# Kernel tuning notes

Measured on AMD Instinct MI355X. Metric: run time of the kernel, lower is better.

## Reference

```python
import jax, jax.numpy as jnp
import numpy as np

B, S, D, HD, P = 4, 8192, 1024, 128, 32
EPS_LN = 1e-5

def setup_inputs() -> dict:
    key = jax.random.key(0)
    ks = jax.random.split(key, 12)
    x      = jax.random.normal(ks[0], (B, S, D), dtype=jnp.float32)
    W_proj = jax.random.normal(ks[1], (8, D, HD), dtype=jnp.float32) * 0.02
    freqs  = jax.random.normal(ks[2], (8, HD), dtype=jnp.float32) * 0.01
    W_pol  = jax.random.normal(ks[3], (8, HD, P), dtype=jnp.float32) * 0.05
    b_pol  = jnp.zeros((8, P), jnp.float32)
    W_imp1 = jax.random.normal(ks[4], (1, 16), dtype=jnp.float32) * 0.5
    b_imp1 = jnp.zeros((16,), jnp.float32)
    W_imp2 = jax.random.normal(ks[5], (16, 1), dtype=jnp.float32) * 0.5
    b_imp2 = jnp.zeros((1,), jnp.float32)
    W_out  = jax.random.normal(ks[6], (D, D), dtype=jnp.float32) * 0.02
    b_out  = jnp.zeros((D,), jnp.float32)
    gamma  = jnp.ones((D,), jnp.float32)
    beta   = jnp.zeros((D,), jnp.float32)
    return dict(x=x, W_proj=W_proj, freqs=freqs, W_pol=W_pol, b_pol=b_pol,
                W_imp1=W_imp1, b_imp1=b_imp1, W_imp2=W_imp2, b_imp2=b_imp2,
                W_out=W_out, b_out=b_out, gamma=gamma, beta=beta)

def reference(x, W_proj, freqs, W_pol, b_pol, W_imp1, b_imp1, W_imp2, b_imp2,
              W_out, b_out, gamma, beta):
    # heads[i] = (x @ W_proj[i]) * cos(pi * freqs[i])   -> (8, B, S, HD)
    heads = jnp.einsum('bsd,hde->hbse', x, W_proj) * jnp.cos(freqs * jnp.pi)[:, None, None, :]

    # --- GuaXiangDuiChong: impedance matrix (B, 8, 8) ---
    hm = heads.mean(axis=2)                                   # (8, B, HD)
    pv = jnp.tanh(jnp.einsum('hbd,hdp->bhp', hm, W_pol) + b_pol[None])  # (B, 8, P)
    pm = pv / jnp.maximum(jnp.linalg.norm(pv, axis=-1, keepdims=True), 1e-12)
    dp = jnp.einsum('bhp,bgp->bhg', pm, pm)                   # (B, 8, 8)
    z = jax.nn.gelu(dp[..., None] * W_imp1[0] + b_imp1, approximate=False)  # (B,8,8,16)
    imp = jax.nn.softplus(jnp.einsum('bhgk,ko->bhgo', z, W_imp2)[..., 0] + b_imp2[0])
    imp = imp * (1.0 - jnp.eye(8, dtype=imp.dtype))           # zero diagonal

    # --- head mixing. Causal masked-mean collapses to row scale (s+1)/S ---
    coeff = (0.1 / (1.0 + imp)) * (1.0 - jnp.eye(8, dtype=imp.dtype))  # (B,8,8), j!=i
    mix = jnp.einsum('big,gbsd->ibsd', coeff, heads)          # (8, B, S, HD)
    causal_scale = (jnp.arange(S, dtype=x.dtype) + 1.0) / S   # (S,)
    out_heads = heads + causal_scale[None, None, :, None] * mix

    merged = out_heads.transpose(1, 2, 0, 3).reshape(B, S, D)
    proj = jnp.einsum('bsd,de->bse', merged, W_out) + b_out   # dropout = identity (eval)
    y = proj + x
    mu = y.mean(axis=-1, keepdims=True)
    var = y.var(axis=-1, keepdims=True)
    y = (y - mu) * jax.lax.rsqrt(var + EPS_LN) * gamma + beta
    return y, imp
```

## Files before the change

kernel.cpp:

```cpp
#include <hip/hip_runtime.h>
#include <hip/hip_bf16.h>
#include <math.h>

typedef __bf16 bf16;
typedef __bf16 bf16x2 __attribute__((ext_vector_type(2)));
typedef __bf16 bf16x4 __attribute__((ext_vector_type(4)));
typedef __bf16 bf16x8 __attribute__((ext_vector_type(8)));
typedef float  f32x4  __attribute__((ext_vector_type(4)));

#define NB 4
#define SS 8192
#define DD 1024
#define MM 32768
#define KK 1024
#define NN 1024
#define NT 16
#define PI_F 3.14159265358979323846f

__device__ __forceinline__ void gl2lds16(const bf16* g, bf16* l) {
    __builtin_amdgcn_global_load_lds(
        (const __attribute__((address_space(1))) void*)g,
        (__attribute__((address_space(3))) void*)l, 16, 0, 0);
}

__global__ __launch_bounds__(256) void prep_x(const float* __restrict__ x,
                                              bf16* __restrict__ xb) {
    size_t i = ((size_t)blockIdx.x * 256 + threadIdx.x) * 4;
    float4 v = *(const float4*)&x[i];
    bf16x4 o;
    o[0] = (bf16)v.x; o[1] = (bf16)v.y; o[2] = (bf16)v.z; o[3] = (bf16)v.w;
    *(bf16x4*)&xb[i] = o;
}

__global__ __launch_bounds__(256) void prep_w(const float* __restrict__ W_proj,
                                              const float* __restrict__ freqs,
                                              const float* __restrict__ W_out,
                                              bf16* __restrict__ WbT1,
                                              bf16* __restrict__ WoT) {
    int idx = blockIdx.x * 256 + threadIdx.x;
    int n = idx >> 10, k = idx & 1023;
    int h = n >> 7, d = n & 127;
    float c = cosf(PI_F * freqs[n]);
    WbT1[idx] = (bf16)(W_proj[(size_t)h * (DD * 128) + (size_t)k * 128 + d] * c);
    WoT[idx]  = (bf16)(W_out[(size_t)k * DD + n]);
}


#define STAGE(G, grow0, kcol, ldsbase)                                        \
    {                                                                         \
        _Pragma("unroll")                                                     \
        for (int i_ = 0; i_ < 2; ++i_) {                                      \
            int p_ = (i_ * 512 + tid) * 16;                                   \
            int lrow_ = p_ >> 7;                                              \
            int cb_ = ((p_ >> 4) & 7) ^ (lrow_ & 7);                          \
            gl2lds16((G) + (size_t)((grow0) + lrow_) * KK + (kcol) + cb_ * 8, \
                     (ldsbase) + i_ * 4096 + w * 512);                        \
        }                                                                     \
    }

#define LDSF(base, row, cbi) \
    (*(const bf16x8*)&(base)[(row) * 64 + ((((cbi) ^ ((row) & 7))) << 3)])

#define READ_A(MQ)                                                            \
    _Pragma("unroll") for (int m_ = 0; m_ < 4; ++m_)                          \
    _Pragma("unroll") for (int ks_ = 0; ks_ < 2; ++ks_)                       \
        a[m_ * 2 + ks_] = LDSF(Ab, wr * 128 + (MQ) * 64 + m_ * 16 + l15, ks_ * 4 + l4);

#define READ_B(NQ, bfr)                                                       \
    _Pragma("unroll") for (int n_ = 0; n_ < 2; ++n_)                          \
    _Pragma("unroll") for (int ks_ = 0; ks_ < 2; ++ks_)                       \
        bfr[n_ * 2 + ks_] = LDSF(Bb, wc * 64 + (NQ) * 32 + n_ * 16 + l15, ks_ * 4 + l4);

#define MFMA_QUAD(MQ, NQ, bfr)                                                \
    _Pragma("unroll") for (int m_ = 0; m_ < 4; ++m_)                          \
    _Pragma("unroll") for (int n_ = 0; n_ < 2; ++n_)                          \
    _Pragma("unroll") for (int ks_ = 0; ks_ < 2; ++ks_)                       \
        acc[(MQ) * 4 + m_][(NQ) * 2 + n_] =                                   \
            __builtin_amdgcn_mfma_f32_16x16x32_bf16(                          \
                a[m_ * 2 + ks_], bfr[n_ * 2 + ks_],                           \
                acc[(MQ) * 4 + m_][(NQ) * 2 + n_], 0, 0, 0);

#define PHASE_BEGIN                                                           \
    __builtin_amdgcn_sched_barrier(0);                                        \
    __builtin_amdgcn_s_barrier();                                             \
    asm volatile("s_waitcnt lgkmcnt(0)" ::: "memory");                        \
    __builtin_amdgcn_sched_barrier(0);                                        \
    __builtin_amdgcn_s_setprio(1);

#define PHASE_END                                                             \
    __builtin_amdgcn_s_setprio(0);                                            \
    __builtin_amdgcn_sched_barrier(0);                                        \
    __builtin_amdgcn_s_barrier();

template <int MODE>
__global__ __launch_bounds__(512, 2)
void gemm256(const bf16* __restrict__ A, const bf16* __restrict__ Bt,
             bf16* __restrict__ Cb, float* __restrict__ Cf,
             const float* __restrict__ bias, const float* __restrict__ resid,
             float* __restrict__ hm) {
    __shared__ bf16 sm[65536];
    const int tid = threadIdx.x;
    const int lane = tid & 63, w = tid >> 6;
    const int wr = w >> 2, wc = w & 3;
    const int l15 = lane & 15, l4 = lane >> 4;

    int wg = blockIdx.x;
    int swz = (wg & 7) * 64 + (wg >> 3);
    const int mt = swz >> 2, ntile = swz & 3;
    const int row0 = mt * 256, col0 = ntile * 256;

    f32x4 acc[8][4] = {};
    bf16x8 a[8], blo[4], bhi[4];

    STAGE(Bt, col0 + 0,   0,  sm + 32768);
    STAGE(Bt, col0 + 128, 0,  sm + 32768 + 8192);
    STAGE(A,  row0 + 0,   0,  sm);
    STAGE(A,  row0 + 128, 0,  sm + 8192);
    STAGE(Bt, col0 + 0,   64, sm + 49152);
    STAGE(Bt, col0 + 128, 64, sm + 49152 + 8192);
    asm volatile("s_waitcnt vmcnt(4)" ::: "memory");
    __builtin_amdgcn_s_barrier();

#pragma unroll 2
    for (int u = 0; u < NT; ++u) {
        const int bo = (u & 1) * 16384;
        bf16* Ab = sm + bo;
        bf16* Bb = sm + 32768 + bo;
        bf16* An = sm + (16384 - bo);
        READ_A(0); READ_B(0, blo);
        if (u + 1 < NT) STAGE(A, row0 + 0, (u + 1) * 64, An);
        PHASE_BEGIN; MFMA_QUAD(0, 0, blo); PHASE_END;
        READ_B(1, bhi);
        if (u + 1 < NT) STAGE(A, row0 + 128, (u + 1) * 64, An + 8192);
        PHASE_BEGIN; MFMA_QUAD(0, 1, bhi); PHASE_END;
        READ_A(1);
        if (u + 2 < NT) STAGE(Bt, col0 + 0, (u + 2) * 64, Bb);
        PHASE_BEGIN; MFMA_QUAD(1, 1, bhi); PHASE_END;
        if (u + 2 < NT) STAGE(Bt, col0 + 128, (u + 2) * 64, Bb + 8192);
        if (u + 2 < NT) { asm volatile("s_waitcnt vmcnt(4)" ::: "memory"); }
        else            { asm volatile("s_waitcnt vmcnt(0)" ::: "memory"); }
        PHASE_BEGIN; MFMA_QUAD(1, 0, blo); PHASE_END;
    }

    if (MODE == 0) {
        const int batch = row0 >> 13;
#pragma unroll
        for (int mg = 0; mg < 8; ++mg) {
            int rbase = row0 + wr * 128 + (mg >> 2) * 64 + (mg & 3) * 16 + l4 * 4;
#pragma unroll
            for (int j = 0; j < 4; ++j) {
                int row = rbase + j;
#pragma unroll
                for (int ng = 0; ng < 4; ++ng) {
                    int col = col0 + wc * 64 + ng * 16 + l15;
                    Cb[(size_t)row * NN + col] = (bf16)acc[mg][ng][j];
                }
            }
        }
#pragma unroll
        for (int ng = 0; ng < 4; ++ng) {
            float s = 0;
#pragma unroll
            for (int mg = 0; mg < 8; ++mg)
#pragma unroll
                for (int j = 0; j < 4; ++j) s += acc[mg][ng][j];
            int col = col0 + wc * 64 + ng * 16 + l15;
            atomicAdd(&hm[batch * DD + col], s);
        }
    } else {
        float bi[4];
#pragma unroll
        for (int ng = 0; ng < 4; ++ng) bi[ng] = bias[col0 + wc * 64 + ng * 16 + l15];
#pragma unroll
        for (int mg = 0; mg < 8; ++mg) {
            int rbase = row0 + wr * 128 + (mg >> 2) * 64 + (mg & 3) * 16 + l4 * 4;
#pragma unroll
            for (int j = 0; j < 4; ++j) {
                size_t row = rbase + j;
#pragma unroll
                for (int ng = 0; ng < 4; ++ng) {
                    int col = col0 + wc * 64 + ng * 16 + l15;
                    Cf[row * NN + col] = acc[mg][ng][j] + bi[ng] + resid[row * NN + col];
                }
            }
        }
    }
}

__global__ __launch_bounds__(1024) void imp_k(const float* __restrict__ hm,
                                              const float* __restrict__ W_pol,
                                              const float* __restrict__ b_pol,
                                              const float* __restrict__ W_imp1,
                                              const float* __restrict__ b_imp1,
                                              const float* __restrict__ W_imp2,
                                              const float* __restrict__ b_imp2,
                                              float* __restrict__ imp_out,
                                              float* __restrict__ coeff) {
    __shared__ float pm_s[32][32];
    int tid = threadIdx.x;
    int bh = tid >> 5, p = tid & 31;
    int b = bh >> 3, h = bh & 7;
    float a = b_pol[h * 32 + p];
    for (int d = 0; d < 128; ++d)
        a += hm[b * DD + h * 128 + d] * (1.0f / SS) * W_pol[(h * 128 + d) * 32 + p];
    float pv = tanhf(a);
    pm_s[bh][p] = pv;
    __syncthreads();
    float ss = 0;
    for (int q = 0; q < 32; ++q) ss += pm_s[bh][q] * pm_s[bh][q];
    float pmv = pv / fmaxf(sqrtf(ss), 1e-12f);
    __syncthreads();
    pm_s[bh][p] = pmv;
    __syncthreads();
    if (tid < 256) {
        int b2 = tid >> 6, h2 = (tid >> 3) & 7, g = tid & 7;
        float dp = 0;
        for (int q = 0; q < 32; ++q) dp += pm_s[b2 * 8 + h2][q] * pm_s[b2 * 8 + g][q];
        float a2 = 0;
        for (int k = 0; k < 16; ++k) {
            float zin = dp * W_imp1[k] + b_imp1[k];
            float zg = 0.5f * zin * (1.0f + erff(zin * 0.70710678118654752f));
            a2 += zg * W_imp2[k];
        }
        float spin = a2 + b_imp2[0];
        float impv = (spin > 20.0f) ? spin : log1pf(expf(spin));
        if (h2 == g) impv = 0.0f;
        imp_out[tid] = impv;
        coeff[tid] = (h2 == g) ? 0.0f : 0.1f / (1.0f + impv);
    }
}

__global__ __launch_bounds__(256) void mix_k(const bf16* __restrict__ heads,
                                             const float* __restrict__ coeff,
                                             bf16* __restrict__ merged) {
    __shared__ float cf[64];
    int tid = threadIdx.x;
    size_t r0 = (size_t)blockIdx.x * 4;
    int b = (int)(r0 >> 13);
    if (tid < 64) cf[tid] = coeff[b * 64 + tid];
    __syncthreads();
    int lr = tid >> 6;
    int d2 = tid & 63;
    size_t r = r0 + lr;
    int s = (int)(r & (SS - 1));
    float cs = (float)(s + 1) * (1.0f / SS);
    const bf16* hrow = heads + r * DD;
    float v0[8], v1[8];
#pragma unroll
    for (int g = 0; g < 8; ++g) {
        bf16x2 v = *(const bf16x2*)&hrow[g * 128 + d2 * 2];
        v0[g] = (float)v[0]; v1[g] = (float)v[1];
    }
    bf16* mrow = merged + r * DD;
#pragma unroll
    for (int h = 0; h < 8; ++h) {
        float a0 = 0, a1 = 0;
#pragma unroll
        for (int g = 0; g < 8; ++g) {
            float c = cf[h * 8 + g];
            a0 += c * v0[g]; a1 += c * v1[g];
        }
        bf16x2 o;
        o[0] = (bf16)(v0[h] + cs * a0);
        o[1] = (bf16)(v1[h] + cs * a1);
        *(bf16x2*)&mrow[h * 128 + d2 * 2] = o;
    }
}

__global__ __launch_bounds__(256) void ln_k(float* __restrict__ y,
                                            const float* __restrict__ gamma,
                                            const float* __restrict__ beta) {
    size_t r = blockIdx.x;
    int tid = threadIdx.x;
    float* row = y + r * DD;
    int e0 = tid * 4;
    float4 v = *(const float4*)&row[e0];
    float sum = v.x + v.y + v.z + v.w;
    float sq  = v.x * v.x + v.y * v.y + v.z * v.z + v.w * v.w;
    for (int off = 32; off > 0; off >>= 1) {
        sum += __shfl_down(sum, off);
        sq  += __shfl_down(sq, off);
    }
    __shared__ float red[8];
    int lane = tid & 63, w = tid >> 6;
    if (lane == 0) { red[w] = sum; red[4 + w] = sq; }
    __syncthreads();
    float tot = red[0] + red[1] + red[2] + red[3];
    float tsq = red[4] + red[5] + red[6] + red[7];
    float mu  = tot * (1.0f / DD);
    float var = tsq * (1.0f / DD) - mu * mu;
    float rs  = rsqrtf(var + 1e-5f);
    float4 g4 = *(const float4*)&gamma[e0];
    float4 b4 = *(const float4*)&beta[e0];
    float4 o;
    o.x = (v.x - mu) * rs * g4.x + b4.x;
    o.y = (v.y - mu) * rs * g4.y + b4.y;
    o.z = (v.z - mu) * rs * g4.z + b4.z;
    o.w = (v.w - mu) * rs * g4.w + b4.w;
    *(float4*)&row[e0] = o;
}

extern "C" void kernel_launch(void* const* d_in, const int* in_sizes, int n_in,
                              void* d_out, int out_size, void* d_ws, size_t ws_size,
                              hipStream_t stream) {
    const float* x      = (const float*)d_in[0];
    const float* W_proj = (const float*)d_in[1];
    const float* freqs  = (const float*)d_in[2];
    const float* W_pol  = (const float*)d_in[3];
    const float* b_pol  = (const float*)d_in[4];
    const float* W_imp1 = (const float*)d_in[5];
    const float* b_imp1 = (const float*)d_in[6];
    const float* W_imp2 = (const float*)d_in[7];
    const float* b_imp2 = (const float*)d_in[8];
    const float* W_out  = (const float*)d_in[9];
    const float* b_out  = (const float*)d_in[10];
    const float* gamma  = (const float*)d_in[11];
    const float* beta   = (const float*)d_in[12];

    char* ws = (char*)d_ws;
    bf16* bufA   = (bf16*)ws;
    bf16* WbT1   = (bf16*)(ws + ((size_t)64 << 20));
    bf16* WoT    = (bf16*)(ws + ((size_t)66 << 20));
    float* hm    = (float*)(ws + ((size_t)68 << 20));
    float* coeff = (float*)(ws + ((size_t)68 << 20) + 16384);

    float* yout = (float*)d_out;
    bf16* heads = (bf16*)d_out;
    float* imp_out = yout + (size_t)MM * DD;

    hipMemsetAsync(hm, 0, NB * DD * sizeof(float), stream);
    prep_x<<<MM * DD / (256 * 4), 256, 0, stream>>>(x, bufA);
    prep_w<<<(NN * KK) / 256, 256, 0, stream>>>(W_proj, freqs, W_out, WbT1, WoT);

    gemm256<0><<<512, 512, 0, stream>>>(bufA, WbT1, heads, nullptr, nullptr, nullptr, hm);

    imp_k<<<1, 1024, 0, stream>>>(hm, W_pol, b_pol, W_imp1, b_imp1, W_imp2, b_imp2,
                                  imp_out, coeff);

    mix_k<<<MM / 4, 256, 0, stream>>>(heads, coeff, bufA);

    gemm256<1><<<512, 512, 0, stream>>>(bufA, WoT, nullptr, yout, b_out, x, nullptr);

    ln_k<<<MM, 256, 0, stream>>>(yout, gamma, beta);
}
```

Baseline: 319.1 us.

## Interleave intermediates in output slots, use bf16 residual/pre-LN, prefetch LDS fragments

Intermediates now live in per-row 4 KB slots inside the output buffer. Heads are stored in the first half, the mixed result in the second half, and the pre-LayerNorm sum goes back into the first half as bf16. The second GEMM reads the bf16 copy of x as its residual instead of fp32 x, and LayerNorm reads bf16 rather than fp32. Together these cut global memory traffic in the later stages. The GEMM main loop is also reordered so the next tile's A/B fragments are read from LDS at the end of each iteration, with vmcnt waits adjusted; this risks synchronization hazards and adds bf16 rounding before LayerNorm.

```diff
diff --git a/kernel.cpp b/kernel.cpp
--- a/kernel.cpp
+++ b/kernel.cpp
@@ -16,6 +16,7 @@
 #define NN 1024
 #define NT 16
 #define PI_F 3.14159265358979323846f
+
 
 __device__ __forceinline__ void gl2lds16(const bf16* g, bf16* l) {
     __builtin_amdgcn_global_load_lds(
@@ -45,59 +46,51 @@
     WoT[idx]  = (bf16)(W_out[(size_t)k * DD + n]);
 }
 
-
-#define STAGE(G, grow0, kcol, ldsbase)                                        \
-    {                                                                         \
-        _Pragma("unroll")                                                     \
-        for (int i_ = 0; i_ < 2; ++i_) {                                      \
-            int p_ = (i_ * 512 + tid) * 16;                                   \
-            int lrow_ = p_ >> 7;                                              \
-            int cb_ = ((p_ >> 4) & 7) ^ (lrow_ & 7);                          \
-            gl2lds16((G) + (size_t)((grow0) + lrow_) * KK + (kcol) + cb_ * 8, \
-                     (ldsbase) + i_ * 4096 + w * 512);                        \
-        }                                                                     \
+#define STAGE(G, grow0, kcol, ldsbase, LDA)                                    \
+    {                                                                          \
+        _Pragma("unroll")                                                      \
+        for (int i_ = 0; i_ < 2; ++i_) {                                       \
+            int p_ = (i_ * 512 + tid) * 16;                                    \
+            int lrow_ = p_ >> 7;                                               \
+            int cb_ = ((p_ >> 4) & 7) ^ (lrow_ & 7);                           \
+            gl2lds16((G) + (size_t)((grow0) + lrow_) * (LDA) + (kcol) + cb_ * 8, \
+                     (ldsbase) + i_ * 4096 + w * 512);                         \
+        }                                                                      \
     }
 
 #define LDSF(base, row, cbi) \
     (*(const bf16x8*)&(base)[(row) * 64 + ((((cbi) ^ ((row) & 7))) << 3)])
 
-#define READ_A(MQ)                                                            \
-    _Pragma("unroll") for (int m_ = 0; m_ < 4; ++m_)                          \
-    _Pragma("unroll") for (int ks_ = 0; ks_ < 2; ++ks_)                       \
-        a[m_ * 2 + ks_] = LDSF(Ab, wr * 128 + (MQ) * 64 + m_ * 16 + l15, ks_ * 4 + l4);
-
-#define READ_B(NQ, bfr)                                                       \
-    _Pragma("unroll") for (int n_ = 0; n_ < 2; ++n_)                          \
-    _Pragma("unroll") for (int ks_ = 0; ks_ < 2; ++ks_)                       \
-        bfr[n_ * 2 + ks_] = LDSF(Bb, wc * 64 + (NQ) * 32 + n_ * 16 + l15, ks_ * 4 + l4);
-
-#define MFMA_QUAD(MQ, NQ, bfr)                                                \
-    _Pragma("unroll") for (int m_ = 0; m_ < 4; ++m_)                          \
-    _Pragma("unroll") for (int n_ = 0; n_ < 2; ++n_)                          \
-    _Pragma("unroll") for (int ks_ = 0; ks_ < 2; ++ks_)                       \
-        acc[(MQ) * 4 + m_][(NQ) * 2 + n_] =                                   \
-            __builtin_amdgcn_mfma_f32_16x16x32_bf16(                          \
-                a[m_ * 2 + ks_], bfr[n_ * 2 + ks_],                           \
-                acc[(MQ) * 4 + m_][(NQ) * 2 + n_], 0, 0, 0);
-
-#define PHASE_BEGIN                                                           \
-    __builtin_amdgcn_sched_barrier(0);                                        \
-    __builtin_amdgcn_s_barrier();                                             \
-    asm volatile("s_waitcnt lgkmcnt(0)" ::: "memory");                        \
-    __builtin_amdgcn_sched_barrier(0);                                        \
-    __builtin_amdgcn_s_setprio(1);
-
-#define PHASE_END                                                             \
-    __builtin_amdgcn_s_setprio(0);                                            \
-    __builtin_amdgcn_sched_barrier(0);                                        \
-    __builtin_amdgcn_s_barrier();
+#define READ_A(MQ, base)                                                       \
+    _Pragma("unroll") for (int m_ = 0; m_ < 4; ++m_)                           \
+    _Pragma("unroll") for (int ks_ = 0; ks_ < 2; ++ks_)                        \
+        a[m_ * 2 + ks_] = LDSF(base, wr * 128 + (MQ) * 64 + m_ * 16 + l15, ks_ * 4 + l4);
+
+#define READ_B(NQ, bfr, base)                                                  \
+    _Pragma("unroll") for (int n_ = 0; n_ < 2; ++n_)                           \
+    _Pragma("unroll") for (int ks_ = 0; ks_ < 2; ++ks_)                        \
+        bfr[n_ * 2 + ks_] = LDSF(base, wc * 64 + (NQ) * 32 + n_ * 16 + l15, ks_ * 4 + l4);
+
+#define MFMA_PH(MQ, NQ, bfr)                                                   \
+    __builtin_amdgcn_s_setprio(1);                                             \
+    _Pragma("unroll") for (int m_ = 0; m_ < 4; ++m_)                           \
+    _Pragma("unroll") for (int n_ = 0; n_ < 2; ++n_)                           \
+    _Pragma("unroll") for (int ks_ = 0; ks_ < 2; ++ks_)                        \
+        acc[(MQ) * 4 + m_][(NQ) * 2 + n_] =                                    \
+            __builtin_amdgcn_mfma_f32_16x16x32_bf16(                           \
+                a[m_ * 2 + ks_], bfr[n_ * 2 + ks_],                            \
+                acc[(MQ) * 4 + m_][(NQ) * 2 + n_], 0, 0, 0);                   \
+    __builtin_amdgcn_s_setprio(0);
+
+#define SCHED0 __builtin_amdgcn_sched_barrier(0)
+#define BAR    SCHED0; __builtin_amdgcn_s_barrier(); SCHED0
+#define LGKM0  asm volatile("s_waitcnt lgkmcnt(0)" ::: "memory"); SCHED0
 
 template <int MODE>
 __global__ __launch_bounds__(512, 2)
-void gemm256(const bf16* __restrict__ A, const bf16* __restrict__ Bt,
-             bf16* __restrict__ Cb, float* __restrict__ Cf,
-             const float* __restrict__ bias, const float* __restrict__ resid,
-             float* __restrict__ hm) {
+void gemm256(const bf16* __restrict__ A, int lda, const bf16* __restrict__ Bt,
+             bf16* __restrict__ Cstr, const bf16* __restrict__ residb,
+             const float* __restrict__ bias, float* __restrict__ hm) {
     __shared__ bf16 sm[65536];
     const int tid = threadIdx.x;
     const int lane = tid & 63, w = tid >> 6;
@@ -112,14 +105,17 @@
     f32x4 acc[8][4] = {};
     bf16x8 a[8], blo[4], bhi[4];
 
-    STAGE(Bt, col0 + 0,   0,  sm + 32768);
-    STAGE(Bt, col0 + 128, 0,  sm + 32768 + 8192);
-    STAGE(A,  row0 + 0,   0,  sm);
-    STAGE(A,  row0 + 128, 0,  sm + 8192);
-    STAGE(Bt, col0 + 0,   64, sm + 49152);
-    STAGE(Bt, col0 + 128, 64, sm + 49152 + 8192);
+    STAGE(Bt, col0 + 0,   0,  sm + 32768,        1024);
+    STAGE(Bt, col0 + 128, 0,  sm + 32768 + 8192, 1024);
+    STAGE(A,  row0 + 0,   0,  sm,                lda);
+    STAGE(A,  row0 + 128, 0,  sm + 8192,         lda);
+    STAGE(Bt, col0 + 0,   64, sm + 49152,        1024);
+    STAGE(Bt, col0 + 128, 64, sm + 49152 + 8192, 1024);
     asm volatile("s_waitcnt vmcnt(4)" ::: "memory");
-    __builtin_amdgcn_s_barrier();
+    BAR;
+    READ_A(0, sm);
+    READ_B(0, blo, (sm + 32768));
+    SCHED0;
 
 #pragma unroll 2
     for (int u = 0; u < NT; ++u) {
@@ -127,19 +123,42 @@
         bf16* Ab = sm + bo;
         bf16* Bb = sm + 32768 + bo;
         bf16* An = sm + (16384 - bo);
-        READ_A(0); READ_B(0, blo);
-        if (u + 1 < NT) STAGE(A, row0 + 0, (u + 1) * 64, An);
-        PHASE_BEGIN; MFMA_QUAD(0, 0, blo); PHASE_END;
-        READ_B(1, bhi);
-        if (u + 1 < NT) STAGE(A, row0 + 128, (u + 1) * 64, An + 8192);
-        PHASE_BEGIN; MFMA_QUAD(0, 1, bhi); PHASE_END;
-        READ_A(1);
-        if (u + 2 < NT) STAGE(Bt, col0 + 0, (u + 2) * 64, Bb);
-        PHASE_BEGIN; MFMA_QUAD(1, 1, bhi); PHASE_END;
-        if (u + 2 < NT) STAGE(Bt, col0 + 128, (u + 2) * 64, Bb + 8192);
-        if (u + 2 < NT) { asm volatile("s_waitcnt vmcnt(4)" ::: "memory"); }
+        bf16* Bn = sm + 32768 + (16384 - bo);
+
+        BAR;
+        if (u + 1 < NT) STAGE(A, row0 + 0, (u + 1) * 64, An, lda);
+        LGKM0;
+        MFMA_PH(0, 0, blo);
+        SCHED0;
+        READ_B(1, bhi, Bb);
+        SCHED0;
+
+        BAR;
+        if (u + 1 < NT) STAGE(A, row0 + 128, (u + 1) * 64, An + 8192, lda);
+        LGKM0;
+        MFMA_PH(0, 1, bhi);
+        SCHED0;
+        READ_A(1, Ab);
+        SCHED0;
+
+        BAR;
+        if (u + 2 < NT) STAGE(Bt, col0 + 0, (u + 2) * 64, Bb, 1024);
+        LGKM0;
+        MFMA_PH(1, 1, bhi);
+        SCHED0;
+        if (u + 2 < NT) { asm volatile("s_waitcnt vmcnt(2)" ::: "memory"); }
         else            { asm volatile("s_waitcnt vmcnt(0)" ::: "memory"); }
-        PHASE_BEGIN; MFMA_QUAD(1, 0, blo); PHASE_END;
+        SCHED0;
+
+        BAR;
+        if (u + 2 < NT) STAGE(Bt, col0 + 128, (u + 2) * 64, Bb + 8192, 1024);
+        MFMA_PH(1, 0, blo);
+        SCHED0;
+        if (u + 1 < NT) {
+            READ_A(0, An);
+            READ_B(0, blo, Bn);
+        }
+        SCHED0;
     }
 
     if (MODE == 0) {
@@ -149,11 +168,11 @@
             int rbase = row0 + wr * 128 + (mg >> 2) * 64 + (mg & 3) * 16 + l4 * 4;
 #pragma unroll
             for (int j = 0; j < 4; ++j) {
-                int row = rbase + j;
+                size_t row = rbase + j;
 #pragma unroll
                 for (int ng = 0; ng < 4; ++ng) {
                     int col = col0 + wc * 64 + ng * 16 + l15;
-                    Cb[(size_t)row * NN + col] = (bf16)acc[mg][ng][j];
+                    Cstr[row * 2048 + col] = (bf16)acc[mg][ng][j];
                 }
             }
         }
@@ -180,7 +199,8 @@
 #pragma unroll
                 for (int ng = 0; ng < 4; ++ng) {
                     int col = col0 + wc * 64 + ng * 16 + l15;
-                    Cf[row * NN + col] = acc[mg][ng][j] + bi[ng] + resid[row * NN + col];
+                    Cstr[row * 2048 + col] =
+                        (bf16)(acc[mg][ng][j] + bi[ng] + (float)residb[row * 1024 + col]);
                 }
             }
         }
@@ -230,9 +250,9 @@
     }
 }
 
-__global__ __launch_bounds__(256) void mix_k(const bf16* __restrict__ heads,
+__global__ __launch_bounds__(256) void mix_k(const char* __restrict__ slots,
                                              const float* __restrict__ coeff,
-                                             bf16* __restrict__ merged) {
+                                             char* __restrict__ slots_w) {
     __shared__ float cf[64];
     int tid = threadIdx.x;
     size_t r0 = (size_t)blockIdx.x * 4;
@@ -244,14 +264,14 @@
     size_t r = r0 + lr;
     int s = (int)(r & (SS - 1));
     float cs = (float)(s + 1) * (1.0f / SS);
-    const bf16* hrow = heads + r * DD;
+    const bf16* hrow = (const bf16*)(slots + r * 4096);
+    bf16* mrow = (bf16*)(slots_w + r * 4096 + 2048);
     float v0[8], v1[8];
 #pragma unroll
     for (int g = 0; g < 8; ++g) {
         bf16x2 v = *(const bf16x2*)&hrow[g * 128 + d2 * 2];
         v0[g] = (float)v[0]; v1[g] = (float)v[1];
     }
-    bf16* mrow = merged + r * DD;
 #pragma unroll
     for (int h = 0; h < 8; ++h) {
         float a0 = 0, a1 = 0;
@@ -267,23 +287,25 @@
     }
 }
 
-__global__ __launch_bounds__(256) void ln_k(float* __restrict__ y,
+__global__ __launch_bounds__(256) void ln_k(char* __restrict__ slots,
                                             const float* __restrict__ gamma,
                                             const float* __restrict__ beta) {
     size_t r = blockIdx.x;
     int tid = threadIdx.x;
-    float* row = y + r * DD;
+    const bf16* zrow = (const bf16*)(slots + r * 4096);
+    float* yrow = (float*)(slots + r * 4096);
     int e0 = tid * 4;
-    float4 v = *(const float4*)&row[e0];
-    float sum = v.x + v.y + v.z + v.w;
-    float sq  = v.x * v.x + v.y * v.y + v.z * v.z + v.w * v.w;
+    bf16x4 zv = *(const bf16x4*)&zrow[e0];
+    float vx = (float)zv[0], vy = (float)zv[1], vz = (float)zv[2], vw = (float)zv[3];
+    float sum = vx + vy + vz + vw;
+    float sq  = vx * vx + vy * vy + vz * vz + vw * vw;
     for (int off = 32; off > 0; off >>= 1) {
         sum += __shfl_down(sum, off);
         sq  += __shfl_down(sq, off);
     }
     __shared__ float red[8];
-    int lane = tid & 63, w = tid >> 6;
-    if (lane == 0) { red[w] = sum; red[4 + w] = sq; }
+    int lane = tid & 63, wv = tid >> 6;
+    if (lane == 0) { red[wv] = sum; red[4 + wv] = sq; }
     __syncthreads();
     float tot = red[0] + red[1] + red[2] + red[3];
     float tsq = red[4] + red[5] + red[6] + red[7];
@@ -293,11 +315,11 @@
     float4 g4 = *(const float4*)&gamma[e0];
     float4 b4 = *(const float4*)&beta[e0];
     float4 o;
-    o.x = (v.x - mu) * rs * g4.x + b4.x;
-    o.y = (v.y - mu) * rs * g4.y + b4.y;
-    o.z = (v.z - mu) * rs * g4.z + b4.z;
-    o.w = (v.w - mu) * rs * g4.w + b4.w;
-    *(float4*)&row[e0] = o;
+    o.x = (vx - mu) * rs * g4.x + b4.x;
+    o.y = (vy - mu) * rs * g4.y + b4.y;
+    o.z = (vz - mu) * rs * g4.z + b4.z;
+    o.w = (vw - mu) * rs * g4.w + b4.w;
+    *(float4*)&yrow[e0] = o;
 }
 
 extern "C" void kernel_launch(void* const* d_in, const int* in_sizes, int n_in,
@@ -318,28 +340,29 @@
     const float* beta   = (const float*)d_in[12];
 
     char* ws = (char*)d_ws;
-    bf16* bufA   = (bf16*)ws;
+    bf16* xb     = (bf16*)ws;
     bf16* WbT1   = (bf16*)(ws + ((size_t)64 << 20));
     bf16* WoT    = (bf16*)(ws + ((size_t)66 << 20));
     float* hm    = (float*)(ws + ((size_t)68 << 20));
     float* coeff = (float*)(ws + ((size_t)68 << 20) + 16384);
 
-    float* yout = (float*)d_out;
-    bf16* heads = (bf16*)d_out;
-    float* imp_out = yout + (size_t)MM * DD;
+    char* slots = (char*)d_out;
+    float* imp_out = (float*)d_out + (size_t)MM * DD;
 
     hipMemsetAsync(hm, 0, NB * DD * sizeof(float), stream);
-    prep_x<<<MM * DD / (256 * 4), 256, 0, stream>>>(x, bufA);
+    prep_x<<<MM * DD / (256 * 4), 256, 0, stream>>>(x, xb);
     prep_w<<<(NN * KK) / 256, 256, 0, stream>>>(W_proj, freqs, W_out, WbT1, WoT);
 
-    gemm256<0><<<512, 512, 0, stream>>>(bufA, WbT1, heads, nullptr, nullptr, nullptr, hm);
+    gemm256<0><<<512, 512, 0, stream>>>(xb, 1024, WbT1, (bf16*)slots,
+                                        nullptr, nullptr, hm);
 
     imp_k<<<1, 1024, 0, stream>>>(hm, W_pol, b_pol, W_imp1, b_imp1, W_imp2, b_imp2,
                                   imp_out, coeff);
 
-    mix_k<<<MM / 4, 256, 0, stream>>>(heads, coeff, bufA);
-
-    gemm256<1><<<512, 512, 0, stream>>>(bufA, WoT, nullptr, yout, b_out, x, nullptr);
-
-    ln_k<<<MM, 256, 0, stream>>>(yout, gamma, beta);
-}
+    mix_k<<<MM / 4, 256, 0, stream>>>(slots, coeff, slots);
+
+    gemm256<1><<<512, 512, 0, stream>>>((const bf16*)slots + 1024, 2048, WoT,
+                                        (bf16*)slots, xb, b_out, nullptr);
+
+    ln_k<<<MM, 256, 0, stream>>>(slots, gamma, beta);
+}
```

Result: faster. 280.6 us (-12.1%).
